# Performance work log

Measured on AMD Instinct MI355X. Metric: run time of the kernel, lower is better.

The kernel has to match this reference:

```python
import jax, jax.numpy as jnp
import numpy as np

N_HEADS = 4

def log_cosh(x):
    # numerically stable log(cosh(x)) = |x| + log1p(exp(-2|x|)) - log(2)
    ax = jnp.abs(x)
    return ax + jnp.log1p(jnp.exp(-2.0 * ax)) - jnp.log(2.0)

def setup_inputs() -> dict:
    key = jax.random.key(0)
    ks = jax.random.split(key, 7)
    B, I, A, E, H = 4, 2048, 2048, 256, N_HEADS
    return {
        "query": jax.random.normal(ks[0], (B, I, E), dtype=jnp.float32),
        "key": jax.random.normal(ks[1], (B, A, E), dtype=jnp.float32),
        "value": jax.random.normal(ks[2], (B, A, E), dtype=jnp.float32),
        "distances": jax.random.uniform(ks[3], (B, I, A), dtype=jnp.float32),
        "in_proj_w": jax.random.normal(ks[4], (3 * E, E), dtype=jnp.float32) * 0.05,
        "out_proj_w": jax.random.normal(ks[5], (E, E), dtype=jnp.float32) * 0.05,
        "mass_w": jax.random.normal(ks[6], (H, E), dtype=jnp.float32) * 0.05,
    }

def reference(query, key, value, distances, in_proj_w, out_proj_w, mass_w):
    B, I, E = query.shape
    A = key.shape[1]
    H = N_HEADS
    D = E // H
    # distance-decay additive bias: mass is (B, A, H), nonnegative via log_cosh
    mass = log_cosh(key @ mass_w.T)                       # (B, A, H)
    bias = jnp.einsum('bah,bia->bhia', -mass, distances)  # (B, H, I, A)
    # nn.MultiheadAttention (bias=False) projections
    wq, wk, wv = jnp.split(in_proj_w, 3, axis=0)          # each (E, E)
    q = (query @ wq.T).reshape(B, I, H, D).transpose(0, 2, 1, 3)  # (B,H,I,D)
    k = (key @ wk.T).reshape(B, A, H, D).transpose(0, 2, 1, 3)    # (B,H,A,D)
    v = (value @ wv.T).reshape(B, A, H, D).transpose(0, 2, 1, 3)  # (B,H,A,D)
    scale = 1.0 / jnp.sqrt(jnp.asarray(D, dtype=q.dtype))
    scores = jnp.einsum('bhid,bhad->bhia', q, k) * scale + bias
    attn = jax.nn.softmax(scores, axis=-1)
    o = jnp.einsum('bhia,bhad->bhid', attn, v)            # (B,H,I,D)
    o = o.transpose(0, 2, 1, 3).reshape(B, I, E)
    return o @ out_proj_w.T
```

## Files before the change

### kernel.cpp

```cpp
#include <hip/hip_runtime.h>
#include <hip/hip_bf16.h>
#include <math.h>

#define BB 4
#define II 2048
#define AA 2048
#define EE 256
#define HH 4

#define LOG2E 1.4426950408889634f
#define SCL   (0.125f * LOG2E)

typedef __bf16 bf16_t;
typedef bf16_t bf16x8 __attribute__((ext_vector_type(8)));
typedef bf16_t bf16x4 __attribute__((ext_vector_type(4)));
typedef float  f32x4  __attribute__((ext_vector_type(4)));

static __device__ __forceinline__ f32x4 mfma16(bf16x8 a, bf16x8 b, f32x4 c) {
    return __builtin_amdgcn_mfma_f32_16x16x32_bf16(a, b, c, 0, 0, 0);
}

static __device__ __forceinline__ void glds16(const bf16_t* g, const bf16_t* l) {
    __builtin_amdgcn_global_load_lds(
        (const __attribute__((address_space(1))) void*)g,
        (__attribute__((address_space(3))) void*)l, 16, 0, 0);
}

static __device__ __forceinline__ void proj_body(
    const float* __restrict__ Aop, const float* __restrict__ Bop,
    bf16_t* __restrict__ Cout, int m0, int n0, int TRANS,
    bf16_t (*sA)[72], bf16_t (*sB)[72])
{
    const int t = threadIdx.x;
    const int w = t >> 6, l = t & 63, g = l >> 4, q = l & 15;
    const int wm = w >> 1, wn = w & 1;
    const int r = t >> 2, s = t & 3;

    f32x4 acc[2][2] = {};

    for (int kt = 0; kt < 4; ++kt) {
        {
            const float* ga = Aop + (size_t)(m0 + r) * EE + kt * 64 + s * 16;
            float tmp[16];
            *(f32x4*)&tmp[0]  = *(const f32x4*)(ga + 0);
            *(f32x4*)&tmp[4]  = *(const f32x4*)(ga + 4);
            *(f32x4*)&tmp[8]  = *(const f32x4*)(ga + 8);
            *(f32x4*)&tmp[12] = *(const f32x4*)(ga + 12);
            bf16x8 w0, w1;
            #pragma unroll
            for (int i = 0; i < 8; ++i) { w0[i] = (bf16_t)tmp[i]; w1[i] = (bf16_t)tmp[8 + i]; }
            *(bf16x8*)&sA[r][s * 16]     = w0;
            *(bf16x8*)&sA[r][s * 16 + 8] = w1;
        }
        {
            const float* gb = Bop + (size_t)(n0 + r) * EE + kt * 64 + s * 16;
            float tmp[16];
            *(f32x4*)&tmp[0]  = *(const f32x4*)(gb + 0);
            *(f32x4*)&tmp[4]  = *(const f32x4*)(gb + 4);
            *(f32x4*)&tmp[8]  = *(const f32x4*)(gb + 8);
            *(f32x4*)&tmp[12] = *(const f32x4*)(gb + 12);
            bf16x8 w0, w1;
            #pragma unroll
            for (int i = 0; i < 8; ++i) { w0[i] = (bf16_t)tmp[i]; w1[i] = (bf16_t)tmp[8 + i]; }
            *(bf16x8*)&sB[r][s * 16]     = w0;
            *(bf16x8*)&sB[r][s * 16 + 8] = w1;
        }
        __syncthreads();
        #pragma unroll
        for (int ks = 0; ks < 2; ++ks) {
            bf16x8 aA[2], aB[2];
            #pragma unroll
            for (int f = 0; f < 2; ++f) {
                aA[f] = *(const bf16x8*)&sA[wm * 32 + f * 16 + q][ks * 32 + g * 8];
                aB[f] = *(const bf16x8*)&sB[wn * 32 + f * 16 + q][ks * 32 + g * 8];
            }
            #pragma unroll
            for (int fm = 0; fm < 2; ++fm)
            #pragma unroll
            for (int fn = 0; fn < 2; ++fn)
                acc[fm][fn] = mfma16(aA[fm], aB[fn], acc[fm][fn]);
        }
        __syncthreads();
    }
    #pragma unroll
    for (int fm = 0; fm < 2; ++fm)
    #pragma unroll
    for (int fn = 0; fn < 2; ++fn)
    #pragma unroll
    for (int j = 0; j < 4; ++j) {
        const int m = m0 + wm * 32 + fm * 16 + g * 4 + j;
        const int n = n0 + wn * 32 + fn * 16 + q;
        const bf16_t v = (bf16_t)acc[fm][fn][j];
        if (TRANS == 0) {
            Cout[(size_t)m * EE + n] = v;
        } else {
            const int bb = n >> 11, a = n & (AA - 1);
            Cout[(size_t)bb * (AA * EE) + (size_t)(a >> 6) * (EE * 64) + m * 64 + (a & 63)] = v;
        }
    }
}

__global__ __launch_bounds__(256) void fused_pre(
    const float* __restrict__ query, const float* __restrict__ key,
    const float* __restrict__ value, const float* __restrict__ in_w,
    const float* __restrict__ mass_w,
    bf16_t* __restrict__ Qp, bf16_t* __restrict__ Kp, bf16_t* __restrict__ Vt,
    float* __restrict__ massT)
{
    __shared__ __align__(16) bf16_t sA[64][72];
    __shared__ __align__(16) bf16_t sB[64][72];
    const int z = blockIdx.z;
    if (z == 0) {
        proj_body(query, in_w, Qp, blockIdx.x * 64, blockIdx.y * 64, 0, sA, sB);
    } else if (z == 1) {
        proj_body(key, in_w + 65536, Kp, blockIdx.x * 64, blockIdx.y * 64, 0, sA, sB);
    } else if (z == 2) {
        proj_body(in_w + 131072, value, Vt, blockIdx.y * 64, blockIdx.x * 64, 1, sA, sB);
    } else {
        const int w = threadIdx.x >> 6, l = threadIdx.x & 63;
        const int p = blockIdx.y * 128 + blockIdx.x;
        const int row0 = p * 16 + w * 4;
        #pragma unroll
        for (int rr = 0; rr < 4; ++rr) {
            const int row = row0 + rr;
            f32x4 kv = *(const f32x4*)(key + (size_t)row * EE + l * 4);
            const int bb = row >> 11, a = row & (AA - 1);
            #pragma unroll
            for (int hh = 0; hh < HH; ++hh) {
                f32x4 mw = *(const f32x4*)(mass_w + hh * EE + l * 4);
                float sdot = kv[0]*mw[0] + kv[1]*mw[1] + kv[2]*mw[2] + kv[3]*mw[3];
                #pragma unroll
                for (int off = 32; off >= 1; off >>= 1) sdot += __shfl_xor(sdot, off, 64);
                if (l == 0) {
                    float ax = fabsf(sdot);
                    massT[((size_t)bb * HH + hh) * AA + a] =
                        (ax + log1pf(__expf(-2.0f * ax)) - 0.693147180559945f) * LOG2E;
                }
            }
        }
    }
}

__global__ __launch_bounds__(256) void out_gemm(
    const bf16_t* __restrict__ Aop, const float* __restrict__ Bop,
    float* __restrict__ Cout)
{
    __shared__ __align__(16) bf16_t sA[64][72];
    __shared__ __align__(16) bf16_t sB[64][72];
    const int t = threadIdx.x;
    const int w = t >> 6, l = t & 63, g = l >> 4, q = l & 15;
    const int wm = w >> 1, wn = w & 1;
    const int m0 = blockIdx.x * 64, n0 = blockIdx.y * 64;
    const int r = t >> 2, s = t & 3;

    f32x4 acc[2][2] = {};

    for (int kt = 0; kt < 4; ++kt) {
        {
            const bf16_t* ga = Aop + (size_t)(m0 + r) * EE + kt * 64 + s * 16;
            *(bf16x8*)&sA[r][s * 16]     = *(const bf16x8*)(ga);
            *(bf16x8*)&sA[r][s * 16 + 8] = *(const bf16x8*)(ga + 8);
        }
        {
            const float* gb = Bop + (size_t)(n0 + r) * EE + kt * 64 + s * 16;
            float tmp[16];
            *(f32x4*)&tmp[0]  = *(const f32x4*)(gb + 0);
            *(f32x4*)&tmp[4]  = *(const f32x4*)(gb + 4);
            *(f32x4*)&tmp[8]  = *(const f32x4*)(gb + 8);
            *(f32x4*)&tmp[12] = *(const f32x4*)(gb + 12);
            bf16x8 w0, w1;
            #pragma unroll
            for (int i = 0; i < 8; ++i) { w0[i] = (bf16_t)tmp[i]; w1[i] = (bf16_t)tmp[8 + i]; }
            *(bf16x8*)&sB[r][s * 16]     = w0;
            *(bf16x8*)&sB[r][s * 16 + 8] = w1;
        }
        __syncthreads();
        #pragma unroll
        for (int ks = 0; ks < 2; ++ks) {
            bf16x8 aA[2], aB[2];
            #pragma unroll
            for (int f = 0; f < 2; ++f) {
                aA[f] = *(const bf16x8*)&sA[wm * 32 + f * 16 + q][ks * 32 + g * 8];
                aB[f] = *(const bf16x8*)&sB[wn * 32 + f * 16 + q][ks * 32 + g * 8];
            }
            #pragma unroll
            for (int fm = 0; fm < 2; ++fm)
            #pragma unroll
            for (int fn = 0; fn < 2; ++fn)
                acc[fm][fn] = mfma16(aA[fm], aB[fn], acc[fm][fn]);
        }
        __syncthreads();
    }
    #pragma unroll
    for (int fm = 0; fm < 2; ++fm)
    #pragma unroll
    for (int fn = 0; fn < 2; ++fn)
    #pragma unroll
    for (int j = 0; j < 4; ++j) {
        const int m = m0 + wm * 32 + fm * 16 + g * 4 + j;
        const int n = n0 + wn * 32 + fn * 16 + q;
        Cout[(size_t)m * EE + n] = acc[fm][fn][j];
    }
}

__global__ __launch_bounds__(512, 4) void attn_kernel(
    const bf16_t* __restrict__ Qp, const bf16_t* __restrict__ Kp,
    const bf16_t* __restrict__ Vt, const float* __restrict__ massT,
    const float* __restrict__ dist, bf16_t* __restrict__ Obuf)
{
    __shared__ __align__(16) bf16_t sK[2][2][4096];
    __shared__ __align__(16) bf16_t sV[2][2][4096];
    __shared__ __align__(16) float  sM[2048];

    const int t = threadIdx.x;
    const int wv = t >> 6, l = t & 63, g = l >> 4, q = l & 15;
    const int s = wv >> 2, rg = wv & 3;
    const int h = blockIdx.y, b = blockIdx.z;
    const int i0 = blockIdx.x * 64;

    *(f32x4*)&sM[t * 4] = *(const f32x4*)(massT + ((size_t)b * HH + h) * AA + t * 4);

    bf16x8 qf[2];
    #pragma unroll
    for (int ks = 0; ks < 2; ++ks)
        qf[ks] = *(const bf16x8*)(Qp + (size_t)(b * II + i0 + rg * 16 + q) * EE
                                     + h * 64 + ks * 32 + g * 8);

    const int u0 = rg * 2;
    const int drow0 = u0 * 8 + (l >> 3);
    const int cc = l & 7;

    auto stage = [&](int a0, int kb) {
        #pragma unroll
        for (int u = 0; u < 2; ++u) {
            const int dr = drow0 + u * 8;
            const int cs = cc ^ (dr & 7);
            glds16(Kp + ((size_t)b * AA + a0 + dr) * EE + h * 64 + cs * 8,
                   &sK[s][kb][(u0 + u) * 512]);
            glds16(Vt + (size_t)b * (AA * EE) + (size_t)(a0 >> 6) * (EE * 64)
                      + (size_t)(h * 64 + dr) * 64 + cs * 8,
                   &sV[s][kb][(u0 + u) * 512]);
        }
    };

    f32x4 rd[4];
    auto load_dist = [&](int a0) {
        const float* gd = dist + ((size_t)b * II + i0 + rg * 16 + q) * AA + a0 + g * 4;
        #pragma unroll
        for (int fa = 0; fa < 4; ++fa) rd[fa] = *(const f32x4*)(gd + fa * 16);
    };

    stage(s * 64, 0);
    load_dist(s * 64);
    __syncthreads();

    float mrun = -INFINITY, lrun = 0.f;
    f32x4 oacc[4] = {};

    for (int k = 0; k < 16; ++k) {
        const int kb = k & 1;
        const int a0 = (2 * k + s) * 64;
        if (k < 15) stage(a0 + 128, kb ^ 1);

        f32x4 st[4] = {};
        __builtin_amdgcn_s_setprio(1);
        #pragma unroll
        for (int fa = 0; fa < 4; ++fa) {
            const int row = fa * 16 + q;
            #pragma unroll
            for (int ks = 0; ks < 2; ++ks) {
                bf16x8 ak = *(const bf16x8*)&sK[s][kb][row * 64 + (((ks * 4 + g) ^ (row & 7)) * 8)];
                st[fa] = mfma16(ak, qf[ks], st[fa]);
            }
        }
        __builtin_amdgcn_s_setprio(0);

        float mloc = -INFINITY;
        #pragma unroll
        for (int fa = 0; fa < 4; ++fa) {
            f32x4 ms = *(const f32x4*)&sM[a0 + fa * 16 + g * 4];
            #pragma unroll
            for (int j = 0; j < 4; ++j) {
                float sv = st[fa][j] * SCL - ms[j] * rd[fa][j];
                st[fa][j] = sv;
                mloc = fmaxf(mloc, sv);
            }
        }
        if (k < 15) load_dist(a0 + 128);

        mloc = fmaxf(mloc, __shfl_xor(mloc, 16, 64));
        mloc = fmaxf(mloc, __shfl_xor(mloc, 32, 64));
        const bool skip = __all(mloc <= mrun);
        float mnew, sc;
        if (skip) { mnew = mrun; sc = 1.f; }
        else { mnew = fmaxf(mrun, mloc); sc = exp2f(mrun - mnew); mrun = mnew; }

        float rs = 0.f;
        #pragma unroll
        for (int fa = 0; fa < 4; ++fa)
        #pragma unroll
        for (int j = 0; j < 4; ++j) {
            float e = exp2f(st[fa][j] - mnew);
            st[fa][j] = e;
            rs += e;
        }
        rs += __shfl_xor(rs, 16, 64);
        rs += __shfl_xor(rs, 32, 64);
        lrun = lrun * sc + rs;

        if (!skip) {
            float osc[4];
            #pragma unroll
            for (int j = 0; j < 4; ++j) osc[j] = __shfl(sc, g * 4 + j, 64);
            #pragma unroll
            for (int fd = 0; fd < 4; ++fd)
            #pragma unroll
            for (int j = 0; j < 4; ++j) oacc[fd][j] *= osc[j];
        }

        bf16x8 pa[2];
        #pragma unroll
        for (int ka = 0; ka < 2; ++ka)
        #pragma unroll
        for (int j = 0; j < 8; ++j)
            pa[ka][j] = (bf16_t)st[2 * ka + (j >> 2)][j & 3];

        __builtin_amdgcn_s_setprio(1);
        #pragma unroll
        for (int ka = 0; ka < 2; ++ka)
        #pragma unroll
        for (int fd = 0; fd < 4; ++fd) {
            const int row = fd * 16 + q;
            const int base = row * 64 + (g & 1) * 4;
            bf16x4 v0 = *(const bf16x4*)&sV[s][kb][base + (((ka * 4 +     (g >> 1)) ^ (row & 7)) * 8)];
            bf16x4 v1 = *(const bf16x4*)&sV[s][kb][base + (((ka * 4 + 2 + (g >> 1)) ^ (row & 7)) * 8)];
            bf16x8 bv;
            #pragma unroll
            for (int j = 0; j < 4; ++j) { bv[j] = v0[j]; bv[4 + j] = v1[j]; }
            oacc[fd] = mfma16(pa[ka], bv, oacc[fd]);
        }
        __builtin_amdgcn_s_setprio(0);

        __syncthreads();
    }

    float* cb = (float*)&sK[0][0][0];
    if (s == 1) {
        float* p = cb + (rg * 64 + l) * 20;
        p[0] = mrun; p[1] = lrun;
        #pragma unroll
        for (int fd = 0; fd < 4; ++fd) *(f32x4*)(p + 2 + fd * 4) = oacc[fd];
    }
    __syncthreads();
    if (s == 0) {
        const float* p = cb + (rg * 64 + l) * 20;
        const float mB = p[0], lB = p[1];
        const float mS = fmaxf(mrun, mB);
        const float aS = exp2f(mrun - mS), bS = exp2f(mB - mS);
        const float lS = lrun * aS + lB * bS;
        float aSo[4], bSo[4], inv[4];
        #pragma unroll
        for (int j = 0; j < 4; ++j) {
            aSo[j] = __shfl(aS, g * 4 + j, 64);
            bSo[j] = __shfl(bS, g * 4 + j, 64);
            inv[j] = 1.0f / __shfl(lS, g * 4 + j, 64);
        }
        #pragma unroll
        for (int fd = 0; fd < 4; ++fd) {
            f32x4 ob = *(const f32x4*)(p + 2 + fd * 4);
            #pragma unroll
            for (int j = 0; j < 4; ++j) {
                const float o = (oacc[fd][j] * aSo[j] + ob[j] * bSo[j]) * inv[j];
                Obuf[(size_t)(b * II + i0 + rg * 16 + g * 4 + j) * EE
                     + h * 64 + fd * 16 + q] = (bf16_t)o;
            }
        }
    }
}

extern "C" void kernel_launch(void* const* d_in, const int* in_sizes, int n_in,
                              void* d_out, int out_size, void* d_ws, size_t ws_size,
                              hipStream_t stream)
{
    const float* query  = (const float*)d_in[0];
    const float* key    = (const float*)d_in[1];
    const float* value  = (const float*)d_in[2];
    const float* dist   = (const float*)d_in[3];
    const float* in_w   = (const float*)d_in[4];
    const float* out_w  = (const float*)d_in[5];
    const float* mass_w = (const float*)d_in[6];
    float* out = (float*)d_out;

    char* ws = (char*)d_ws;
    bf16_t* Qp    = (bf16_t*)(ws);
    bf16_t* Kp    = (bf16_t*)(ws + 1 * 4194304);
    bf16_t* Vt    = (bf16_t*)(ws + 2 * 4194304);
    bf16_t* Obuf  = (bf16_t*)(ws + 3 * 4194304);
    float*  massT = (float*) (ws + 4 * 4194304);

    fused_pre<<<dim3(128, 4, 4), dim3(256), 0, stream>>>(
        query, key, value, in_w, mass_w, Qp, Kp, Vt, massT);
    attn_kernel<<<dim3(32, 4, 4), dim3(512), 0, stream>>>(Qp, Kp, Vt, massT, dist, Obuf);
    out_gemm<<<dim3(128, 4), dim3(256), 0, stream>>>(Obuf, out_w, out);
}
```

Before: 91.96 us.

## Fold score scale into Q, lazy rescale, MFMA row sums, permuted V layout

Folds the softmax scale and log2e into the Q projection output, which removes a multiply per score. The online softmax now rescales only when the running max grows by more than 8 (a lazy threshold), and row sums are accumulated with an MFMA against a ones vector instead of shuffle reductions. V is stored with a permuted column order so each PV operand is a single 8-wide LDS load instead of two 4-wide loads. Global pointers advance incrementally, and the mass projection loads its weights once and batches the four head reductions. The lazy threshold lets exp values reach up to 2^8 before rescaling, which adds some bf16/fp32 range risk.

Measured after the change: 81.59 us. 1.13x faster.

```diff
diff --git a/kernel.cpp b/kernel.cpp
--- a/kernel.cpp
+++ b/kernel.cpp
@@ -28,7 +28,7 @@
 
 static __device__ __forceinline__ void proj_body(
     const float* __restrict__ Aop, const float* __restrict__ Bop,
-    bf16_t* __restrict__ Cout, int m0, int n0, int TRANS,
+    bf16_t* __restrict__ Cout, int m0, int n0, int TRANS, float cscale,
     bf16_t (*sA)[72], bf16_t (*sB)[72])
 {
     const int t = threadIdx.x;
@@ -90,12 +90,14 @@
     for (int j = 0; j < 4; ++j) {
         const int m = m0 + wm * 32 + fm * 16 + g * 4 + j;
         const int n = n0 + wn * 32 + fn * 16 + q;
-        const bf16_t v = (bf16_t)acc[fm][fn][j];
+        const bf16_t v = (bf16_t)(acc[fm][fn][j] * cscale);
         if (TRANS == 0) {
             Cout[(size_t)m * EE + n] = v;
         } else {
             const int bb = n >> 11, a = n & (AA - 1);
-            Cout[(size_t)bb * (AA * EE) + (size_t)(a >> 6) * (EE * 64) + m * 64 + (a & 63)] = v;
+            const int a6 = a & 63;
+            const int p6 = (a6 & 32) | ((a6 & 12) << 1) | ((a6 & 16) >> 2) | (a6 & 3);
+            Cout[(size_t)bb * (AA * EE) + (size_t)(a >> 6) * (EE * 64) + m * 64 + p6] = v;
         }
     }
 }
@@ -111,28 +113,37 @@
     __shared__ __align__(16) bf16_t sB[64][72];
     const int z = blockIdx.z;
     if (z == 0) {
-        proj_body(query, in_w, Qp, blockIdx.x * 64, blockIdx.y * 64, 0, sA, sB);
+        proj_body(query, in_w, Qp, blockIdx.x * 64, blockIdx.y * 64, 0, SCL, sA, sB);
     } else if (z == 1) {
-        proj_body(key, in_w + 65536, Kp, blockIdx.x * 64, blockIdx.y * 64, 0, sA, sB);
+        proj_body(key, in_w + 65536, Kp, blockIdx.x * 64, blockIdx.y * 64, 0, 1.0f, sA, sB);
     } else if (z == 2) {
-        proj_body(in_w + 131072, value, Vt, blockIdx.y * 64, blockIdx.x * 64, 1, sA, sB);
+        proj_body(in_w + 131072, value, Vt, blockIdx.y * 64, blockIdx.x * 64, 1, 1.0f, sA, sB);
     } else {
         const int w = threadIdx.x >> 6, l = threadIdx.x & 63;
         const int p = blockIdx.y * 128 + blockIdx.x;
         const int row0 = p * 16 + w * 4;
+        f32x4 mw[HH];
+        #pragma unroll
+        for (int hh = 0; hh < HH; ++hh)
+            mw[hh] = *(const f32x4*)(mass_w + hh * EE + l * 4);
         #pragma unroll
         for (int rr = 0; rr < 4; ++rr) {
             const int row = row0 + rr;
             f32x4 kv = *(const f32x4*)(key + (size_t)row * EE + l * 4);
-            const int bb = row >> 11, a = row & (AA - 1);
-            #pragma unroll
-            for (int hh = 0; hh < HH; ++hh) {
-                f32x4 mw = *(const f32x4*)(mass_w + hh * EE + l * 4);
-                float sdot = kv[0]*mw[0] + kv[1]*mw[1] + kv[2]*mw[2] + kv[3]*mw[3];
+            f32x4 sd;
+            #pragma unroll
+            for (int hh = 0; hh < HH; ++hh)
+                sd[hh] = kv[0]*mw[hh][0] + kv[1]*mw[hh][1] + kv[2]*mw[hh][2] + kv[3]*mw[hh][3];
+            #pragma unroll
+            for (int off = 32; off >= 1; off >>= 1) {
                 #pragma unroll
-                for (int off = 32; off >= 1; off >>= 1) sdot += __shfl_xor(sdot, off, 64);
-                if (l == 0) {
-                    float ax = fabsf(sdot);
+                for (int hh = 0; hh < HH; ++hh) sd[hh] += __shfl_xor(sd[hh], off, 64);
+            }
+            if (l == 0) {
+                const int bb = row >> 11, a = row & (AA - 1);
+                #pragma unroll
+                for (int hh = 0; hh < HH; ++hh) {
+                    float ax = fabsf(sd[hh]);
                     massT[((size_t)bb * HH + hh) * AA + a] =
                         (ax + log1pf(__expf(-2.0f * ax)) - 0.693147180559945f) * LOG2E;
                 }
@@ -228,39 +239,49 @@
 
     const int u0 = rg * 2;
     const int drow0 = u0 * 8 + (l >> 3);
-    const int cc = l & 7;
-
-    auto stage = [&](int a0, int kb) {
+    const int cs = (l & 7) ^ (drow0 & 7);
+
+    const bf16_t* pkg = Kp + ((size_t)b * AA + s * 64 + drow0) * EE + h * 64 + cs * 8;
+    const bf16_t* pvg = Vt + (size_t)b * (AA * EE) + (size_t)s * (EE * 64)
+                           + (size_t)(h * 64 + drow0) * 64 + cs * 8;
+    const float*  pdg = dist + ((size_t)b * II + i0 + rg * 16 + q) * AA + s * 64 + g * 4;
+
+    auto stage = [&](int kb) {
         #pragma unroll
         for (int u = 0; u < 2; ++u) {
-            const int dr = drow0 + u * 8;
-            const int cs = cc ^ (dr & 7);
-            glds16(Kp + ((size_t)b * AA + a0 + dr) * EE + h * 64 + cs * 8,
-                   &sK[s][kb][(u0 + u) * 512]);
-            glds16(Vt + (size_t)b * (AA * EE) + (size_t)(a0 >> 6) * (EE * 64)
-                      + (size_t)(h * 64 + dr) * 64 + cs * 8,
-                   &sV[s][kb][(u0 + u) * 512]);
+            glds16(pkg + u * (8 * EE), &sK[s][kb][(u0 + u) * 512]);
+            glds16(pvg + u * (8 * 64), &sV[s][kb][(u0 + u) * 512]);
         }
     };
 
     f32x4 rd[4];
-    auto load_dist = [&](int a0) {
-        const float* gd = dist + ((size_t)b * II + i0 + rg * 16 + q) * AA + a0 + g * 4;
-        #pragma unroll
-        for (int fa = 0; fa < 4; ++fa) rd[fa] = *(const f32x4*)(gd + fa * 16);
+    auto load_dist = [&]() {
+        #pragma unroll
+        for (int fa = 0; fa < 4; ++fa) rd[fa] = *(const f32x4*)(pdg + fa * 16);
     };
 
-    stage(s * 64, 0);
-    load_dist(s * 64);
+    stage(0);
+    pkg += 128 * EE; pvg += 2 * (EE * 64);
+    load_dist();
+    pdg += 128;
     __syncthreads();
 
-    float mrun = -INFINITY, lrun = 0.f;
+    float mrun = -INFINITY;
     f32x4 oacc[4] = {};
-
+    f32x4 lacc = {};
+    bf16x8 vone;
+    #pragma unroll
+    for (int j = 0; j < 8; ++j) vone[j] = (bf16_t)1.0f;
+
+    int ma = s * 64;
+
+    #pragma unroll 2
     for (int k = 0; k < 16; ++k) {
         const int kb = k & 1;
-        const int a0 = (2 * k + s) * 64;
-        if (k < 15) stage(a0 + 128, kb ^ 1);
+        if (k < 15) {
+            stage(kb ^ 1);
+            pkg += 128 * EE; pvg += 2 * (EE * 64);
+        }
 
         f32x4 st[4] = {};
         __builtin_amdgcn_s_setprio(1);
@@ -278,45 +299,41 @@
         float mloc = -INFINITY;
         #pragma unroll
         for (int fa = 0; fa < 4; ++fa) {
-            f32x4 ms = *(const f32x4*)&sM[a0 + fa * 16 + g * 4];
+            f32x4 ms = *(const f32x4*)&sM[ma + fa * 16 + g * 4];
             #pragma unroll
             for (int j = 0; j < 4; ++j) {
-                float sv = st[fa][j] * SCL - ms[j] * rd[fa][j];
+                float sv = fmaf(-ms[j], rd[fa][j], st[fa][j]);
                 st[fa][j] = sv;
                 mloc = fmaxf(mloc, sv);
             }
         }
-        if (k < 15) load_dist(a0 + 128);
+        ma += 128;
+        if (k < 15) { load_dist(); pdg += 128; }
 
         mloc = fmaxf(mloc, __shfl_xor(mloc, 16, 64));
         mloc = fmaxf(mloc, __shfl_xor(mloc, 32, 64));
-        const bool skip = __all(mloc <= mrun);
-        float mnew, sc;
-        if (skip) { mnew = mrun; sc = 1.f; }
-        else { mnew = fmaxf(mrun, mloc); sc = exp2f(mrun - mnew); mrun = mnew; }
-
-        float rs = 0.f;
+        const bool skip = __all(mloc <= mrun + 8.0f);
+        float mnew = mrun;
+        if (!skip) {
+            mnew = fmaxf(mrun, mloc);
+            const float sc = exp2f(mrun - mnew);
+            mrun = mnew;
+            float osc[4];
+            #pragma unroll
+            for (int j = 0; j < 4; ++j) osc[j] = __shfl(sc, g * 4 + j, 64);
+            #pragma unroll
+            for (int fd = 0; fd < 4; ++fd)
+            #pragma unroll
+            for (int j = 0; j < 4; ++j) oacc[fd][j] *= osc[j];
+            #pragma unroll
+            for (int j = 0; j < 4; ++j) lacc[j] *= osc[j];
+        }
+
         #pragma unroll
         for (int fa = 0; fa < 4; ++fa)
         #pragma unroll
-        for (int j = 0; j < 4; ++j) {
-            float e = exp2f(st[fa][j] - mnew);
-            st[fa][j] = e;
-            rs += e;
-        }
-        rs += __shfl_xor(rs, 16, 64);
-        rs += __shfl_xor(rs, 32, 64);
-        lrun = lrun * sc + rs;
-
-        if (!skip) {
-            float osc[4];
-            #pragma unroll
-            for (int j = 0; j < 4; ++j) osc[j] = __shfl(sc, g * 4 + j, 64);
-            #pragma unroll
-            for (int fd = 0; fd < 4; ++fd)
-            #pragma unroll
-            for (int j = 0; j < 4; ++j) oacc[fd][j] *= osc[j];
-        }
+        for (int j = 0; j < 4; ++j)
+            st[fa][j] = exp2f(st[fa][j] - mnew);
 
         bf16x8 pa[2];
         #pragma unroll
@@ -327,17 +344,14 @@
 
         __builtin_amdgcn_s_setprio(1);
         #pragma unroll
-        for (int ka = 0; ka < 2; ++ka)
-        #pragma unroll
-        for (int fd = 0; fd < 4; ++fd) {
-            const int row = fd * 16 + q;
-            const int base = row * 64 + (g & 1) * 4;
-            bf16x4 v0 = *(const bf16x4*)&sV[s][kb][base + (((ka * 4 +     (g >> 1)) ^ (row & 7)) * 8)];
-            bf16x4 v1 = *(const bf16x4*)&sV[s][kb][base + (((ka * 4 + 2 + (g >> 1)) ^ (row & 7)) * 8)];
-            bf16x8 bv;
-            #pragma unroll
-            for (int j = 0; j < 4; ++j) { bv[j] = v0[j]; bv[4 + j] = v1[j]; }
-            oacc[fd] = mfma16(pa[ka], bv, oacc[fd]);
+        for (int ka = 0; ka < 2; ++ka) {
+            #pragma unroll
+            for (int fd = 0; fd < 4; ++fd) {
+                const int row = fd * 16 + q;
+                bf16x8 bv = *(const bf16x8*)&sV[s][kb][row * 64 + (((ka * 4 + g) ^ (row & 7)) * 8)];
+                oacc[fd] = mfma16(pa[ka], bv, oacc[fd]);
+            }
+            lacc = mfma16(pa[ka], vone, lacc);
         }
         __builtin_amdgcn_s_setprio(0);
 
@@ -346,28 +360,31 @@
 
     float* cb = (float*)&sK[0][0][0];
     if (s == 1) {
-        float* p = cb + (rg * 64 + l) * 20;
-        p[0] = mrun; p[1] = lrun;
-        #pragma unroll
-        for (int fd = 0; fd < 4; ++fd) *(f32x4*)(p + 2 + fd * 4) = oacc[fd];
+        float* p = cb + (rg * 64 + l) * 24;
+        p[0] = mrun;
+        *(f32x4*)(p + 4) = lacc;
+        #pragma unroll
+        for (int fd = 0; fd < 4; ++fd) *(f32x4*)(p + 8 + fd * 4) = oacc[fd];
     }
     __syncthreads();
     if (s == 0) {
-        const float* p = cb + (rg * 64 + l) * 20;
-        const float mB = p[0], lB = p[1];
+        const float* p = cb + (rg * 64 + l) * 24;
+        const float mB = p[0];
+        const f32x4 lB = *(const f32x4*)(p + 4);
         const float mS = fmaxf(mrun, mB);
         const float aS = exp2f(mrun - mS), bS = exp2f(mB - mS);
-        const float lS = lrun * aS + lB * bS;
         float aSo[4], bSo[4], inv[4];
         #pragma unroll
         for (int j = 0; j < 4; ++j) {
             aSo[j] = __shfl(aS, g * 4 + j, 64);
             bSo[j] = __shfl(bS, g * 4 + j, 64);
-            inv[j] = 1.0f / __shfl(lS, g * 4 + j, 64);
-        }
+        }
+        #pragma unroll
+        for (int j = 0; j < 4; ++j)
+            inv[j] = 1.0f / (lacc[j] * aSo[j] + lB[j] * bSo[j]);
         #pragma unroll
         for (int fd = 0; fd < 4; ++fd) {
-            f32x4 ob = *(const f32x4*)(p + 2 + fd * 4);
+            f32x4 ob = *(const f32x4*)(p + 8 + fd * 4);
             #pragma unroll
             for (int j = 0; j < 4; ++j) {
                 const float o = (oacc[fd][j] * aSo[j] + ob[j] * bSo[j]) * inv[j];
```
